# Kernel tuning notes

Hardware: AMD Instinct MI355X
Metric: run time of the kernel (lower is better)

Reference implementation:

```python
import jax, jax.numpy as jnp
import numpy as np

B, S, D, H = 2, 2048, 1024, 16
DH = D // H  # d_head = 64


def setup_inputs() -> dict:
    key = jax.random.key(0)
    ks = jax.random.split(key, 12)
    s = 1.0 / np.sqrt(D)
    inp = {
        "Q": jax.random.normal(ks[0], (B, S, D), dtype=jnp.float32),
        "K": jax.random.normal(ks[1], (B, S, D), dtype=jnp.float32),
        "V": jax.random.normal(ks[2], (B, S, D), dtype=jnp.float32),
        "attn_mask": jax.random.randint(ks[3], (B, 1, S, S), 0, 2) > 0,
        "Wq": jax.random.normal(ks[4], (D, D), dtype=jnp.float32) * s,
        "bq": jnp.zeros((D,), dtype=jnp.float32),
        "Wk": jax.random.normal(ks[5], (D, D), dtype=jnp.float32) * s,
        "bk": jnp.zeros((D,), dtype=jnp.float32),
        "Wv": jax.random.normal(ks[6], (D, D), dtype=jnp.float32) * s,
        "bv": jnp.zeros((D,), dtype=jnp.float32),
        "Wo": jax.random.normal(ks[7], (D, D), dtype=jnp.float32) * s,
        "bo": jnp.zeros((D,), dtype=jnp.float32),
    }
    return inp


def reference(Q, K, V, attn_mask, Wq, bq, Wk, bk, Wv, bv, Wo, bo):
    # QKV projections -> [B, H, S, DH]
    def proj(x, W, b):
        return (x @ W + b).reshape(B, S, H, DH).transpose(0, 2, 1, 3)

    q = proj(Q, Wq, bq)
    k = proj(K, Wk, bk)
    v = proj(V, Wv, bv)

    # scaled dot-product attention with boolean masked_fill(-1e9)
    scores = jnp.einsum("bhqd,bhkd->bhqk", q, k) / jnp.sqrt(jnp.float32(DH))
    scores = jnp.where(attn_mask, jnp.float32(-1e9), scores)
    soft_mat = jax.nn.softmax(scores, axis=-1)          # [B, H, S, S]
    attn = jnp.einsum("bhqk,bhkd->bhqd", soft_mat, v)   # [B, H, S, DH]

    # concat heads + output projection
    concat = attn.transpose(0, 2, 1, 3).reshape(B, S, D)
    output = concat @ Wo + bo
    return (output, soft_mat)
```

## Files before the change

### kernel.cpp

```cpp
#include <hip/hip_runtime.h>

#define BB 2
#define SS 2048
#define DD 1024
#define HH 16
#define DHH 64

typedef float v4f __attribute__((ext_vector_type(4)));
typedef short v8s __attribute__((ext_vector_type(8)));

__device__ __forceinline__ unsigned short f2bf(float f) {
  unsigned u = __float_as_uint(f);
  u += 0x7FFFu + ((u >> 16) & 1u);
  return (unsigned short)(u >> 16);
}

__global__ void k_detect(const unsigned* mw, int* flag) {
  __shared__ unsigned red[256];
  int t = threadIdx.x;
  unsigned bits = 0;
  for (int i = t; i < 1024; i += 256) {
    unsigned w = mw[i];
    if (w & 0xFFFFFF00u) bits |= 2u;
    if (w == 0x3F800000u) bits |= 1u;
  }
  red[t] = bits;
  __syncthreads();
  for (int s = 128; s > 0; s >>= 1) {
    if (t < s) red[t] |= red[t + s];
    __syncthreads();
  }
  if (t == 0) {
    unsigned b = red[0];
    int fmt = 0;
    if (b & 2u) fmt = (b & 1u) ? 2 : 1;
    *flag = fmt;
  }
}

__global__ void k_pack(const void* mask, unsigned long long* packed, const int* flag) {
  int fmt = *flag;
  long long gid = (long long)blockIdx.x * 256 + threadIdx.x;
  bool pred;
  if (fmt == 0)      pred = ((const int*)mask)[gid] != 0;
  else if (fmt == 1) pred = ((const unsigned char*)mask)[gid] != 0;
  else               pred = ((const float*)mask)[gid] > 0.0f;
  unsigned long long bal = __ballot(pred);
  if ((threadIdx.x & 63) == 0) packed[gid >> 6] = bal;
}

__global__ void k_wtrans(const float* W0, const float* W1, const float* W2, const float* W3,
                         unsigned short* WT) {
  const float* W = blockIdx.z == 0 ? W0 : blockIdx.z == 1 ? W1 : blockIdx.z == 2 ? W2 : W3;
  unsigned short* o = WT + (size_t)blockIdx.z * DD * DD;
  __shared__ float tile[32][33];
  int x = threadIdx.x, y = threadIdx.y;
  int n0 = blockIdx.x * 32, k0 = blockIdx.y * 32;
#pragma unroll
  for (int j = 0; j < 4; ++j)
    tile[y + 8 * j][x] = W[(size_t)(k0 + y + 8 * j) * DD + n0 + x];
  __syncthreads();
#pragma unroll
  for (int j = 0; j < 4; ++j)
    o[(size_t)(n0 + y + 8 * j) * DD + k0 + x] = f2bf(tile[x][y + 8 * j]);
}

__launch_bounds__(256)
__global__ void k_proj(const float* Q, const float* K, const float* V,
                       const unsigned short* WT,
                       const float* bq, const float* bk, const float* bv,
                       unsigned short* qh, unsigned short* kh, unsigned short* vh) {
  int z = blockIdx.z;
  const float* X = z == 0 ? Q : z == 1 ? K : V;
  const unsigned short* Wt = WT + (size_t)z * DD * DD;
  const float* bias = z == 0 ? bq : z == 1 ? bk : bv;
  unsigned short* out = z == 0 ? qh : z == 1 ? kh : vh;

  __shared__ __align__(16) char As[128 * 32 * 2];
  __shared__ __align__(16) char Bs[128 * 32 * 2];

  int tid = threadIdx.x;
  int lane = tid & 63, wv = tid >> 6;
  int wr = wv >> 1, wc = wv & 1;
  int g = lane >> 4, r = lane & 15;

  v4f vz = {0.f, 0.f, 0.f, 0.f};
  v4f acc[4][4];
#pragma unroll
  for (int m = 0; m < 4; ++m)
#pragma unroll
    for (int n = 0; n < 4; ++n) acc[m][n] = vz;

  int srow = tid >> 1;
  int shalf = tid & 1;
  const float* aptr = X + (size_t)(blockIdx.x * 128 + srow) * DD + shalf * 16;
  const unsigned short* bptr = Wt + (size_t)(blockIdx.y * 128 + srow) * DD + shalf * 16;
  unsigned sbase = srow * 64 + shalf * 32;
  unsigned sxor = (srow & 7) << 4;

  for (int k0 = 0; k0 < DD; k0 += 32) {
    const float4* a4 = (const float4*)(aptr + k0);
    float4 f0 = a4[0], f1 = a4[1], f2 = a4[2], f3 = a4[3];
    v8s pa0, pa1;
    pa0[0] = (short)f2bf(f0.x); pa0[1] = (short)f2bf(f0.y);
    pa0[2] = (short)f2bf(f0.z); pa0[3] = (short)f2bf(f0.w);
    pa0[4] = (short)f2bf(f1.x); pa0[5] = (short)f2bf(f1.y);
    pa0[6] = (short)f2bf(f1.z); pa0[7] = (short)f2bf(f1.w);
    pa1[0] = (short)f2bf(f2.x); pa1[1] = (short)f2bf(f2.y);
    pa1[2] = (short)f2bf(f2.z); pa1[3] = (short)f2bf(f2.w);
    pa1[4] = (short)f2bf(f3.x); pa1[5] = (short)f2bf(f3.y);
    pa1[6] = (short)f2bf(f3.z); pa1[7] = (short)f2bf(f3.w);
    v8s pb0 = *(const v8s*)(bptr + k0);
    v8s pb1 = *(const v8s*)(bptr + k0 + 8);
    __syncthreads();
    *(v8s*)(As + ((sbase + 0) ^ sxor)) = pa0;
    *(v8s*)(As + ((sbase + 16) ^ sxor)) = pa1;
    *(v8s*)(Bs + ((sbase + 0) ^ sxor)) = pb0;
    *(v8s*)(Bs + ((sbase + 16) ^ sxor)) = pb1;
    __syncthreads();
    v8s af[4], bf_[4];
#pragma unroll
    for (int m = 0; m < 4; ++m) {
      int row = wr * 64 + m * 16 + r;
      af[m] = *(const v8s*)(As + ((row * 64 + g * 16) ^ ((r & 7) << 4)));
    }
#pragma unroll
    for (int n = 0; n < 4; ++n) {
      int row = wc * 64 + n * 16 + r;
      bf_[n] = *(const v8s*)(Bs + ((row * 64 + g * 16) ^ ((r & 7) << 4)));
    }
#pragma unroll
    for (int m = 0; m < 4; ++m)
#pragma unroll
      for (int n = 0; n < 4; ++n)
        acc[m][n] = __builtin_amdgcn_mfma_f32_16x16x32_bf16(af[m], bf_[n], acc[m][n], 0, 0, 0);
  }

#pragma unroll
  for (int n = 0; n < 4; ++n) {
    int nglob = blockIdx.y * 128 + wc * 64 + n * 16 + r;
    float bsv = bias[nglob];
    int h = nglob >> 6, dh = nglob & 63;
#pragma unroll
    for (int m = 0; m < 4; ++m) {
#pragma unroll
      for (int i = 0; i < 4; ++i) {
        int mglob = blockIdx.x * 128 + wr * 64 + m * 16 + g * 4 + i;
        int b = mglob >> 11, s = mglob & 2047;
        out[(((size_t)(b * HH + h) * SS + s) << 6) + dh] = f2bf(acc[m][n][i] + bsv);
      }
    }
  }
}

__launch_bounds__(512)
__global__ void k_attn(const unsigned short* qh, const unsigned short* kh,
                       const unsigned short* vh, const unsigned* packed,
                       float* soft_out, unsigned short* attn_out) {
  __shared__ __align__(16) char smem[148480];
  float* sc = (float*)smem;
  float* part = (float*)(smem + 65536);
  unsigned short* Vt = (unsigned short*)(smem + 131072);

  int tid = threadIdx.x;
  int lane = tid & 63, wv = tid >> 6;
  int g = lane >> 4, r = lane & 15;
  int qb = blockIdx.x, h = blockIdx.y, b = blockIdx.z;
  int qbase = qb << 4;
  size_t hoff = ((size_t)(b * HH + h)) * SS * DHH;
  const unsigned short* qp = qh + hoff;
  const unsigned short* kp = kh + hoff;
  const unsigned short* vp = vh + hoff;

  v8s aq[2];
#pragma unroll
  for (int ks = 0; ks < 2; ++ks)
    aq[ks] = *(const v8s*)(qp + (size_t)(qbase + r) * 64 + ks * 32 + g * 8);
  int n0w = wv << 8;
  for (int nt = 0; nt < 16; ++nt) {
    int n0 = n0w + (nt << 4);
    v4f acc = {0.f, 0.f, 0.f, 0.f};
#pragma unroll
    for (int ks = 0; ks < 2; ++ks) {
      v8s bfr = *(const v8s*)(kp + (size_t)(n0 + r) * 64 + ks * 32 + g * 8);
      acc = __builtin_amdgcn_mfma_f32_16x16x32_bf16(aq[ks], bfr, acc, 0, 0, 0);
    }
#pragma unroll
    for (int i = 0; i < 4; ++i)
      sc[(g * 4 + i) * 2048 + n0 + r] = acc[i];
  }
  __syncthreads();

  float4 e[2][8];
  float inv[2];
#pragma unroll
  for (int rr = 0; rr < 2; ++rr) {
    int row = wv * 2 + rr;
    const unsigned* mrow = packed + ((size_t)b * SS + qbase + row) * 64;
    float4 s4[8];
    float mx = -3.0e38f;
#pragma unroll
    for (int j = 0; j < 8; ++j) {
      int ki = j * 256 + lane * 4;
      float4 v = *(const float4*)(sc + row * 2048 + ki);
      unsigned w = mrow[8 * j + (lane >> 3)];
      unsigned sh = (lane & 7) * 4;
      v.x = ((w >> (sh + 0)) & 1u) ? -1e9f : v.x * 0.125f;
      v.y = ((w >> (sh + 1)) & 1u) ? -1e9f : v.y * 0.125f;
      v.z = ((w >> (sh + 2)) & 1u) ? -1e9f : v.z * 0.125f;
      v.w = ((w >> (sh + 3)) & 1u) ? -1e9f : v.w * 0.125f;
      s4[j] = v;
      mx = fmaxf(mx, fmaxf(fmaxf(v.x, v.y), fmaxf(v.z, v.w)));
    }
#pragma unroll
    for (int off = 32; off >= 1; off >>= 1)
      mx = fmaxf(mx, __shfl_xor(mx, off));
    float sum = 0.f;
#pragma unroll
    for (int j = 0; j < 8; ++j) {
      float4 ev;
      ev.x = __expf(s4[j].x - mx);
      ev.y = __expf(s4[j].y - mx);
      ev.z = __expf(s4[j].z - mx);
      ev.w = __expf(s4[j].w - mx);
      e[rr][j] = ev;
      sum += (ev.x + ev.y) + (ev.z + ev.w);
    }
#pragma unroll
    for (int off = 32; off >= 1; off >>= 1)
      sum += __shfl_xor(sum, off);
    float iv = 1.0f / sum;
    inv[rr] = iv;
    float* op = soft_out + ((size_t)(b * HH + h) * SS + qbase + row) * SS;
#pragma unroll
    for (int j = 0; j < 8; ++j) {
      float4 pv;
      pv.x = e[rr][j].x * iv;
      pv.y = e[rr][j].y * iv;
      pv.z = e[rr][j].z * iv;
      pv.w = e[rr][j].w * iv;
      *(float4*)(op + j * 256 + lane * 4) = pv;
    }
  }
  __syncthreads();

#pragma unroll
  for (int rr = 0; rr < 2; ++rr) {
    int row = wv * 2 + rr;
    float iv = inv[rr];
    unsigned rx = (row & 7) << 4;
#pragma unroll
    for (int j = 0; j < 8; ++j) {
      int ki = j * 256 + lane * 4;
      ushort4 pk;
      pk.x = f2bf(e[rr][j].x * iv);
      pk.y = f2bf(e[rr][j].y * iv);
      pk.z = f2bf(e[rr][j].z * iv);
      pk.w = f2bf(e[rr][j].w * iv);
      *(ushort4*)(smem + ((unsigned)(row * 4096 + ki * 2) ^ rx)) = pk;
    }
  }

  int ksw = wv & 3, ng = wv >> 2;
  v4f vz = {0.f, 0.f, 0.f, 0.f};
  v4f pacc[2];
  pacc[0] = vz; pacc[1] = vz;
  int vr = tid >> 2;
  int vd0 = (tid & 3) << 4;
  for (int c = 0; c < 16; ++c) {
    __syncthreads();
    const unsigned short* vsrc = vp + (size_t)(c * 128 + vr) * 64 + vd0;
    v8s v0 = *(const v8s*)(vsrc);
    v8s v1 = *(const v8s*)(vsrc + 8);
#pragma unroll
    for (int i = 0; i < 8; ++i) Vt[(vd0 + i) * 136 + vr] = (unsigned short)v0[i];
#pragma unroll
    for (int i = 0; i < 8; ++i) Vt[(vd0 + 8 + i) * 136 + vr] = (unsigned short)v1[i];
    __syncthreads();
    unsigned paddr = (unsigned)(r * 4096 + c * 256 + ksw * 64 + g * 16);
    paddr ^= (unsigned)((r & 7) << 4);
    v8s pa = *(const v8s*)(smem + paddr);
#pragma unroll
    for (int t = 0; t < 2; ++t) {
      int n = ((ng * 2 + t) << 4) + r;
      v8s vb = *(const v8s*)(Vt + n * 136 + ksw * 32 + g * 8);
      pacc[t] = __builtin_amdgcn_mfma_f32_16x16x32_bf16(pa, vb, pacc[t], 0, 0, 0);
    }
  }

#pragma unroll
  for (int t = 0; t < 2; ++t)
#pragma unroll
    for (int i = 0; i < 4; ++i)
      part[((wv * 2 + t) * 16 + g * 4 + i) * 16 + r] = pacc[t][i];
  __syncthreads();
  for (int o = tid; o < 1024; o += 512) {
    int m = o >> 6, col = o & 63;
    int grp = col >> 5, tt = (col >> 4) & 1, cc = col & 15;
    float v = 0.f;
#pragma unroll
    for (int k4 = 0; k4 < 4; ++k4)
      v += part[(((grp * 4 + k4) * 2 + tt) * 16 + m) * 16 + cc];
    attn_out[((size_t)b * SS + qbase + m) * DD + (h << 6) + col] = f2bf(v);
  }
}

__launch_bounds__(256)
__global__ void k_oproj(const unsigned short* A, const unsigned short* WT4,
                        const float* bo, float* out) {
  const unsigned short* Wt = WT4 + (size_t)3 * DD * DD;
  __shared__ __align__(16) char As[128 * 32 * 2];
  __shared__ __align__(16) char Bs[128 * 32 * 2];

  int tid = threadIdx.x;
  int lane = tid & 63, wv = tid >> 6;
  int wr = wv >> 1, wc = wv & 1;
  int g = lane >> 4, r = lane & 15;

  v4f vz = {0.f, 0.f, 0.f, 0.f};
  v4f acc[4][4];
#pragma unroll
  for (int m = 0; m < 4; ++m)
#pragma unroll
    for (int n = 0; n < 4; ++n) acc[m][n] = vz;

  int srow = tid >> 1;
  int shalf = tid & 1;
  const unsigned short* aptr = A + (size_t)(blockIdx.x * 128 + srow) * DD + shalf * 16;
  const unsigned short* bptr = Wt + (size_t)(blockIdx.y * 128 + srow) * DD + shalf * 16;
  unsigned sbase = srow * 64 + shalf * 32;
  unsigned sxor = (srow & 7) << 4;

  for (int k0 = 0; k0 < DD; k0 += 32) {
    v8s pa0 = *(const v8s*)(aptr + k0);
    v8s pa1 = *(const v8s*)(aptr + k0 + 8);
    v8s pb0 = *(const v8s*)(bptr + k0);
    v8s pb1 = *(const v8s*)(bptr + k0 + 8);
    __syncthreads();
    *(v8s*)(As + ((sbase + 0) ^ sxor)) = pa0;
    *(v8s*)(As + ((sbase + 16) ^ sxor)) = pa1;
    *(v8s*)(Bs + ((sbase + 0) ^ sxor)) = pb0;
    *(v8s*)(Bs + ((sbase + 16) ^ sxor)) = pb1;
    __syncthreads();
    v8s af[4], bf_[4];
#pragma unroll
    for (int m = 0; m < 4; ++m) {
      int row = wr * 64 + m * 16 + r;
      af[m] = *(const v8s*)(As + ((row * 64 + g * 16) ^ ((r & 7) << 4)));
    }
#pragma unroll
    for (int n = 0; n < 4; ++n) {
      int row = wc * 64 + n * 16 + r;
      bf_[n] = *(const v8s*)(Bs + ((row * 64 + g * 16) ^ ((r & 7) << 4)));
    }
#pragma unroll
    for (int m = 0; m < 4; ++m)
#pragma unroll
      for (int n = 0; n < 4; ++n)
        acc[m][n] = __builtin_amdgcn_mfma_f32_16x16x32_bf16(af[m], bf_[n], acc[m][n], 0, 0, 0);
  }

#pragma unroll
  for (int n = 0; n < 4; ++n) {
    int nglob = blockIdx.y * 128 + wc * 64 + n * 16 + r;
    float bsv = bo[nglob];
#pragma unroll
    for (int m = 0; m < 4; ++m) {
#pragma unroll
      for (int i = 0; i < 4; ++i) {
        int mglob = blockIdx.x * 128 + wr * 64 + m * 16 + g * 4 + i;
        out[(size_t)mglob * DD + nglob] = acc[m][n][i] + bsv;
      }
    }
  }
}

extern "C" void kernel_launch(void* const* d_in, const int* in_sizes, int n_in,
                              void* d_out, int out_size, void* d_ws, size_t ws_size,
                              hipStream_t stream) {
  (void)in_sizes; (void)n_in; (void)out_size; (void)ws_size;
  const float* Q  = (const float*)d_in[0];
  const float* K  = (const float*)d_in[1];
  const float* V  = (const float*)d_in[2];
  const void*  M  = d_in[3];
  const float* Wq = (const float*)d_in[4];
  const float* bq = (const float*)d_in[5];
  const float* Wk = (const float*)d_in[6];
  const float* bk = (const float*)d_in[7];
  const float* Wv = (const float*)d_in[8];
  const float* bv = (const float*)d_in[9];
  const float* Wo = (const float*)d_in[10];
  const float* bo = (const float*)d_in[11];

  float* out  = (float*)d_out;
  float* soft = out + (size_t)BB * SS * DD;

  char* ws = (char*)d_ws;
  int* flag = (int*)ws;
  unsigned long long* packed = (unsigned long long*)(ws + 256);
  unsigned short* WT   = (unsigned short*)(ws + 256 + 1048576);
  unsigned short* qhp  = (unsigned short*)(ws + 256 + 1048576 + 8388608);
  unsigned short* khp  = qhp + (size_t)BB * SS * DD;
  unsigned short* vhp  = khp + (size_t)BB * SS * DD;
  unsigned short* attn = vhp + (size_t)BB * SS * DD;

  k_detect<<<1, 256, 0, stream>>>((const unsigned*)M, flag);
  k_pack<<<BB * SS * SS / 256, 256, 0, stream>>>(M, packed, flag);
  k_wtrans<<<dim3(32, 32, 4), dim3(32, 8), 0, stream>>>(Wq, Wk, Wv, Wo, WT);
  k_proj<<<dim3(32, 8, 3), 256, 0, stream>>>(Q, K, V, WT, bq, bk, bv, qhp, khp, vhp);
  k_attn<<<dim3(SS / 16, HH, BB), 512, 0, stream>>>(qhp, khp, vhp, (const unsigned*)packed, soft, attn);
  k_oproj<<<dim3(32, 8), 256, 0, stream>>>(attn, WT, bo, out);
}
```

Baseline: 1.142 ms.

## Keep attention scores in registers and store V pre-transposed from projection

The projection kernel now writes V in a transposed [b,h,dh,s] layout, so the attention kernel reads V directly from global memory instead of transposing it through shared memory in every chunk. The score tile is computed as K·Qᵀ and held in registers, and the softmax is done in registers with cross-wave reductions through a small shared buffer, replacing the fp32 score staging in LDS. The P·V product splits the key range over two wave halves and sums the two partials. Shared memory per block drops from about 145KB to about 74KB, and launch bounds ask for higher occupancy, at the cost of more registers per thread and strided V reads.

```diff
diff --git a/kernel.cpp b/kernel.cpp
--- a/kernel.cpp
+++ b/kernel.cpp
@@ -69,12 +69,12 @@
 __global__ void k_proj(const float* Q, const float* K, const float* V,
                        const unsigned short* WT,
                        const float* bq, const float* bk, const float* bv,
-                       unsigned short* qh, unsigned short* kh, unsigned short* vh) {
+                       unsigned short* qh, unsigned short* kh, unsigned short* vhT) {
   int z = blockIdx.z;
   const float* X = z == 0 ? Q : z == 1 ? K : V;
   const unsigned short* Wt = WT + (size_t)z * DD * DD;
   const float* bias = z == 0 ? bq : z == 1 ? bk : bv;
-  unsigned short* out = z == 0 ? qh : z == 1 ? kh : vh;
+  unsigned short* out = z == 0 ? qh : z == 1 ? kh : vhT;
 
   __shared__ __align__(16) char As[128 * 32 * 2];
   __shared__ __align__(16) char Bs[128 * 32 * 2];
@@ -136,172 +136,162 @@
         acc[m][n] = __builtin_amdgcn_mfma_f32_16x16x32_bf16(af[m], bf_[n], acc[m][n], 0, 0, 0);
   }
 
-#pragma unroll
-  for (int n = 0; n < 4; ++n) {
-    int nglob = blockIdx.y * 128 + wc * 64 + n * 16 + r;
-    float bsv = bias[nglob];
-    int h = nglob >> 6, dh = nglob & 63;
-#pragma unroll
-    for (int m = 0; m < 4; ++m) {
-#pragma unroll
-      for (int i = 0; i < 4; ++i) {
-        int mglob = blockIdx.x * 128 + wr * 64 + m * 16 + g * 4 + i;
-        int b = mglob >> 11, s = mglob & 2047;
-        out[(((size_t)(b * HH + h) * SS + s) << 6) + dh] = f2bf(acc[m][n][i] + bsv);
+  if (z == 2) {
+#pragma unroll
+    for (int n = 0; n < 4; ++n) {
+      int nglob = blockIdx.y * 128 + wc * 64 + n * 16 + r;
+      float bsv = bias[nglob];
+      int h = nglob >> 6, dh = nglob & 63;
+#pragma unroll
+      for (int m = 0; m < 4; ++m) {
+        int mg0 = blockIdx.x * 128 + wr * 64 + m * 16 + g * 4;
+        int b0 = mg0 >> 11, s0 = mg0 & 2047;
+        ushort4 pk;
+        pk.x = f2bf(acc[m][n][0] + bsv);
+        pk.y = f2bf(acc[m][n][1] + bsv);
+        pk.z = f2bf(acc[m][n][2] + bsv);
+        pk.w = f2bf(acc[m][n][3] + bsv);
+        *(ushort4*)(out + ((size_t)(b0 * HH + h) * DHH + dh) * SS + s0) = pk;
       }
     }
-  }
-}
-
-__launch_bounds__(512)
+  } else {
+#pragma unroll
+    for (int n = 0; n < 4; ++n) {
+      int nglob = blockIdx.y * 128 + wc * 64 + n * 16 + r;
+      float bsv = bias[nglob];
+      int h = nglob >> 6, dh = nglob & 63;
+#pragma unroll
+      for (int m = 0; m < 4; ++m) {
+#pragma unroll
+        for (int i = 0; i < 4; ++i) {
+          int mglob = blockIdx.x * 128 + wr * 64 + m * 16 + g * 4 + i;
+          int b0 = mglob >> 11, s0 = mglob & 2047;
+          out[(((size_t)(b0 * HH + h) * SS + s0) << 6) + dh] = f2bf(acc[m][n][i] + bsv);
+        }
+      }
+    }
+  }
+}
+
+__launch_bounds__(512, 4)
 __global__ void k_attn(const unsigned short* qh, const unsigned short* kh,
-                       const unsigned short* vh, const unsigned* packed,
+                       const unsigned short* vhT, const unsigned* packed,
                        float* soft_out, unsigned short* attn_out) {
-  __shared__ __align__(16) char smem[148480];
-  float* sc = (float*)smem;
-  float* part = (float*)(smem + 65536);
-  unsigned short* Vt = (unsigned short*)(smem + 131072);
+  __shared__ __align__(16) char Pb[65536];
+  __shared__ float red[2][8][16];
+  __shared__ float red2[4][16][16];
 
   int tid = threadIdx.x;
   int lane = tid & 63, wv = tid >> 6;
   int g = lane >> 4, r = lane & 15;
   int qb = blockIdx.x, h = blockIdx.y, b = blockIdx.z;
   int qbase = qb << 4;
-  size_t hoff = ((size_t)(b * HH + h)) * SS * DHH;
+  int bh = b * HH + h;
+  size_t hoff = (size_t)bh * SS * DHH;
   const unsigned short* qp = qh + hoff;
   const unsigned short* kp = kh + hoff;
-  const unsigned short* vp = vh + hoff;
-
-  v8s aq[2];
+  int n0w = wv << 8;
+
+  v8s bqf[2];
 #pragma unroll
   for (int ks = 0; ks < 2; ++ks)
-    aq[ks] = *(const v8s*)(qp + (size_t)(qbase + r) * 64 + ks * 32 + g * 8);
-  int n0w = wv << 8;
+    bqf[ks] = *(const v8s*)(qp + (size_t)(qbase + r) * 64 + ks * 32 + g * 8);
+
+  v4f acc[16];
+#pragma unroll
   for (int nt = 0; nt < 16; ++nt) {
-    int n0 = n0w + (nt << 4);
-    v4f acc = {0.f, 0.f, 0.f, 0.f};
+    const unsigned short* krow = kp + (size_t)(n0w + nt * 16 + r) * 64;
+    v4f a = {0.f, 0.f, 0.f, 0.f};
 #pragma unroll
     for (int ks = 0; ks < 2; ++ks) {
-      v8s bfr = *(const v8s*)(kp + (size_t)(n0 + r) * 64 + ks * 32 + g * 8);
-      acc = __builtin_amdgcn_mfma_f32_16x16x32_bf16(aq[ks], bfr, acc, 0, 0, 0);
-    }
-#pragma unroll
-    for (int i = 0; i < 4; ++i)
-      sc[(g * 4 + i) * 2048 + n0 + r] = acc[i];
-  }
-  __syncthreads();
-
-  float4 e[2][8];
-  float inv[2];
-#pragma unroll
-  for (int rr = 0; rr < 2; ++rr) {
-    int row = wv * 2 + rr;
-    const unsigned* mrow = packed + ((size_t)b * SS + qbase + row) * 64;
-    float4 s4[8];
-    float mx = -3.0e38f;
-#pragma unroll
-    for (int j = 0; j < 8; ++j) {
-      int ki = j * 256 + lane * 4;
-      float4 v = *(const float4*)(sc + row * 2048 + ki);
-      unsigned w = mrow[8 * j + (lane >> 3)];
-      unsigned sh = (lane & 7) * 4;
-      v.x = ((w >> (sh + 0)) & 1u) ? -1e9f : v.x * 0.125f;
-      v.y = ((w >> (sh + 1)) & 1u) ? -1e9f : v.y * 0.125f;
-      v.z = ((w >> (sh + 2)) & 1u) ? -1e9f : v.z * 0.125f;
-      v.w = ((w >> (sh + 3)) & 1u) ? -1e9f : v.w * 0.125f;
-      s4[j] = v;
-      mx = fmaxf(mx, fmaxf(fmaxf(v.x, v.y), fmaxf(v.z, v.w)));
-    }
-#pragma unroll
-    for (int off = 32; off >= 1; off >>= 1)
-      mx = fmaxf(mx, __shfl_xor(mx, off));
-    float sum = 0.f;
-#pragma unroll
-    for (int j = 0; j < 8; ++j) {
-      float4 ev;
-      ev.x = __expf(s4[j].x - mx);
-      ev.y = __expf(s4[j].y - mx);
-      ev.z = __expf(s4[j].z - mx);
-      ev.w = __expf(s4[j].w - mx);
-      e[rr][j] = ev;
-      sum += (ev.x + ev.y) + (ev.z + ev.w);
-    }
-#pragma unroll
-    for (int off = 32; off >= 1; off >>= 1)
-      sum += __shfl_xor(sum, off);
-    float iv = 1.0f / sum;
-    inv[rr] = iv;
-    float* op = soft_out + ((size_t)(b * HH + h) * SS + qbase + row) * SS;
-#pragma unroll
-    for (int j = 0; j < 8; ++j) {
-      float4 pv;
-      pv.x = e[rr][j].x * iv;
-      pv.y = e[rr][j].y * iv;
-      pv.z = e[rr][j].z * iv;
-      pv.w = e[rr][j].w * iv;
-      *(float4*)(op + j * 256 + lane * 4) = pv;
-    }
-  }
-  __syncthreads();
-
-#pragma unroll
-  for (int rr = 0; rr < 2; ++rr) {
-    int row = wv * 2 + rr;
-    float iv = inv[rr];
-    unsigned rx = (row & 7) << 4;
-#pragma unroll
-    for (int j = 0; j < 8; ++j) {
-      int ki = j * 256 + lane * 4;
-      ushort4 pk;
-      pk.x = f2bf(e[rr][j].x * iv);
-      pk.y = f2bf(e[rr][j].y * iv);
-      pk.z = f2bf(e[rr][j].z * iv);
-      pk.w = f2bf(e[rr][j].w * iv);
-      *(ushort4*)(smem + ((unsigned)(row * 4096 + ki * 2) ^ rx)) = pk;
-    }
-  }
-
-  int ksw = wv & 3, ng = wv >> 2;
-  v4f vz = {0.f, 0.f, 0.f, 0.f};
-  v4f pacc[2];
-  pacc[0] = vz; pacc[1] = vz;
-  int vr = tid >> 2;
-  int vd0 = (tid & 3) << 4;
-  for (int c = 0; c < 16; ++c) {
-    __syncthreads();
-    const unsigned short* vsrc = vp + (size_t)(c * 128 + vr) * 64 + vd0;
-    v8s v0 = *(const v8s*)(vsrc);
-    v8s v1 = *(const v8s*)(vsrc + 8);
-#pragma unroll
-    for (int i = 0; i < 8; ++i) Vt[(vd0 + i) * 136 + vr] = (unsigned short)v0[i];
-#pragma unroll
-    for (int i = 0; i < 8; ++i) Vt[(vd0 + 8 + i) * 136 + vr] = (unsigned short)v1[i];
-    __syncthreads();
-    unsigned paddr = (unsigned)(r * 4096 + c * 256 + ksw * 64 + g * 16);
-    paddr ^= (unsigned)((r & 7) << 4);
-    v8s pa = *(const v8s*)(smem + paddr);
-#pragma unroll
-    for (int t = 0; t < 2; ++t) {
-      int n = ((ng * 2 + t) << 4) + r;
-      v8s vb = *(const v8s*)(Vt + n * 136 + ksw * 32 + g * 8);
-      pacc[t] = __builtin_amdgcn_mfma_f32_16x16x32_bf16(pa, vb, pacc[t], 0, 0, 0);
-    }
-  }
-
-#pragma unroll
-  for (int t = 0; t < 2; ++t)
-#pragma unroll
-    for (int i = 0; i < 4; ++i)
-      part[((wv * 2 + t) * 16 + g * 4 + i) * 16 + r] = pacc[t][i];
-  __syncthreads();
-  for (int o = tid; o < 1024; o += 512) {
-    int m = o >> 6, col = o & 63;
-    int grp = col >> 5, tt = (col >> 4) & 1, cc = col & 15;
-    float v = 0.f;
-#pragma unroll
-    for (int k4 = 0; k4 < 4; ++k4)
-      v += part[(((grp * 4 + k4) * 2 + tt) * 16 + m) * 16 + cc];
-    attn_out[((size_t)b * SS + qbase + m) * DD + (h << 6) + col] = f2bf(v);
+      v8s av = *(const v8s*)(krow + ks * 32 + g * 8);
+      a = __builtin_amdgcn_mfma_f32_16x16x32_bf16(av, bqf[ks], a, 0, 0, 0);
+    }
+    acc[nt] = a;
+  }
+
+  const uint4* mb = (const uint4*)((const char*)packed + ((size_t)b * SS + qbase + r) * 256 + wv * 32);
+  uint4 mAw = mb[0], mBw = mb[1];
+  unsigned w8[8] = {mAw.x, mAw.y, mAw.z, mAw.w, mBw.x, mBw.y, mBw.z, mBw.w};
+
+  float mx = -3.0e38f;
+#pragma unroll
+  for (int nt = 0; nt < 16; ++nt) {
+    unsigned w = w8[nt >> 1];
+    unsigned sh0 = (nt & 1) * 16 + g * 4;
+#pragma unroll
+    for (int i = 0; i < 4; ++i) {
+      float s = ((w >> (sh0 + i)) & 1u) ? -1e9f : acc[nt][i] * 0.125f;
+      acc[nt][i] = s;
+      mx = fmaxf(mx, s);
+    }
+  }
+  mx = fmaxf(mx, __shfl_xor(mx, 16));
+  mx = fmaxf(mx, __shfl_xor(mx, 32));
+  if (lane < 16) red[0][wv][lane] = mx;
+  __syncthreads();
+  float gmx = red[0][0][r];
+#pragma unroll
+  for (int j = 1; j < 8; ++j) gmx = fmaxf(gmx, red[0][j][r]);
+
+  float sum = 0.f;
+#pragma unroll
+  for (int nt = 0; nt < 16; ++nt) {
+#pragma unroll
+    for (int i = 0; i < 4; ++i) {
+      float e = __expf(acc[nt][i] - gmx);
+      acc[nt][i] = e;
+      sum += e;
+    }
+  }
+  sum += __shfl_xor(sum, 16);
+  sum += __shfl_xor(sum, 32);
+  if (lane < 16) red[1][wv][lane] = sum;
+  __syncthreads();
+  float gs = 0.f;
+#pragma unroll
+  for (int j = 0; j < 8; ++j) gs += red[1][j][r];
+  float inv = 1.0f / gs;
+
+  float* op = soft_out + ((size_t)bh * SS + qbase + r) * SS + n0w;
+#pragma unroll
+  for (int nt = 0; nt < 16; ++nt) {
+    float4 pv;
+    pv.x = acc[nt][0] * inv;
+    pv.y = acc[nt][1] * inv;
+    pv.z = acc[nt][2] * inv;
+    pv.w = acc[nt][3] * inv;
+    *(float4*)(op + nt * 16 + g * 4) = pv;
+    unsigned lo = ((unsigned)f2bf(pv.y) << 16) | (unsigned)f2bf(pv.x);
+    unsigned hi = ((unsigned)f2bf(pv.w) << 16) | (unsigned)f2bf(pv.z);
+    unsigned addr = (unsigned)(r * 4096 + (n0w + nt * 16 + g * 4) * 2) ^ ((unsigned)(r & 7) << 4);
+    *(uint2*)(Pb + addr) = make_uint2(lo, hi);
+  }
+  __syncthreads();
+
+  int ng = wv & 3, hf = wv >> 2;
+  const unsigned short* vt = vhT + ((size_t)bh * DHH + ng * 16 + r) * SS;
+  v4f pacc = {0.f, 0.f, 0.f, 0.f};
+#pragma unroll 4
+  for (int c = 0; c < 32; ++c) {
+    int kb = hf * 1024 + c * 32;
+    unsigned paddr = (unsigned)(r * 4096 + kb * 2 + g * 16) ^ ((unsigned)(r & 7) << 4);
+    v8s pa = *(const v8s*)(Pb + paddr);
+    v8s vb = *(const v8s*)(vt + kb + g * 8);
+    pacc = __builtin_amdgcn_mfma_f32_16x16x32_bf16(pa, vb, pacc, 0, 0, 0);
+  }
+
+  if (hf) {
+#pragma unroll
+    for (int i = 0; i < 4; ++i) red2[ng][g * 4 + i][r] = pacc[i];
+  }
+  __syncthreads();
+  if (!hf) {
+#pragma unroll
+    for (int i = 0; i < 4; ++i) {
+      float s = pacc[i] + red2[ng][g * 4 + i][r];
+      attn_out[((size_t)b * SS + qbase + g * 4 + i) * DD + h * 64 + ng * 16 + r] = f2bf(s);
+    }
   }
 }
 
@@ -401,13 +391,13 @@
   unsigned short* WT   = (unsigned short*)(ws + 256 + 1048576);
   unsigned short* qhp  = (unsigned short*)(ws + 256 + 1048576 + 8388608);
   unsigned short* khp  = qhp + (size_t)BB * SS * DD;
-  unsigned short* vhp  = khp + (size_t)BB * SS * DD;
-  unsigned short* attn = vhp + (size_t)BB * SS * DD;
+  unsigned short* vhT  = khp + (size_t)BB * SS * DD;
+  unsigned short* attn = vhT + (size_t)BB * SS * DD;
 
   k_detect<<<1, 256, 0, stream>>>((const unsigned*)M, flag);
   k_pack<<<BB * SS * SS / 256, 256, 0, stream>>>(M, packed, flag);
   k_wtrans<<<dim3(32, 32, 4), dim3(32, 8), 0, stream>>>(Wq, Wk, Wv, Wo, WT);
-  k_proj<<<dim3(32, 8, 3), 256, 0, stream>>>(Q, K, V, WT, bq, bk, bv, qhp, khp, vhp);
-  k_attn<<<dim3(SS / 16, HH, BB), 512, 0, stream>>>(qhp, khp, vhp, (const unsigned*)packed, soft, attn);
+  k_proj<<<dim3(32, 8, 3), 256, 0, stream>>>(Q, K, V, WT, bq, bk, bv, qhp, khp, vhT);
+  k_attn<<<dim3(SS / 16, HH, BB), 512, 0, stream>>>(qhp, khp, vhT, (const unsigned*)packed, soft, attn);
   k_oproj<<<dim3(32, 8), 256, 0, stream>>>(attn, WT, bo, out);
 }
```

Result: faster. 1.011 ms (-11.4%).
